# Performance work log

Hardware: AMD Instinct MI355X
Metric: run time of the kernel (lower is better)

Reference implementation:

```python
import jax, jax.numpy as jnp
import numpy as np

B, L, DIM, H = 2, 2048, 1024, 16
HD = DIM // H  # 64
EPS = 1e-6
ROPE_THETA = 10000.0


def _rmsnorm(x, scale):
    # mean of squares in float32 as in torch (dtype=torch.float32)
    ms = jnp.mean(jnp.square(x.astype(jnp.float32)), axis=-1, keepdims=True)
    inv = jax.lax.rsqrt(ms + EPS).astype(x.dtype)
    return x * inv * scale.astype(x.dtype)


def _rope_cos_sin(seq_len, head_dim, dtype):
    inv_freq = 1.0 / (ROPE_THETA ** (jnp.arange(0, head_dim, 2, dtype=jnp.float32) / head_dim))
    ang = jnp.arange(seq_len, dtype=jnp.float32)[:, None] * inv_freq[None, :]  # [L, HD/2]
    cos = jnp.cos(ang)[:, None, :].astype(dtype)  # [L,1,HD/2] broadcast over heads
    sin = jnp.sin(ang)[:, None, :].astype(dtype)
    return cos, sin


def _rope_apply(x, cos, sin):
    # x: [B,L,H,HD]; rotate-half formulation
    x1, x2 = jnp.split(x, 2, axis=-1)
    return jnp.concatenate([x1 * cos - x2 * sin, x2 * cos + x1 * sin], axis=-1)


def setup_inputs() -> dict:
    key = jax.random.key(0)
    k1, k2, k3 = jax.random.split(key, 3)
    x = jax.random.normal(k1, (B, L, DIM), dtype=jnp.float32)
    Wqkv = jax.random.normal(k2, (DIM, 3 * DIM), dtype=jnp.float32) * (DIM ** -0.5)
    Wproj = jax.random.normal(k3, (DIM, DIM), dtype=jnp.float32) * (DIM ** -0.5)
    q_scale = jnp.ones((HD,), dtype=jnp.float32)
    k_scale = jnp.ones((HD,), dtype=jnp.float32)
    bproj = jnp.zeros((DIM,), dtype=jnp.float32)
    return {"x": x, "Wqkv": Wqkv, "q_scale": q_scale, "k_scale": k_scale,
            "Wproj": Wproj, "bproj": bproj}


def reference(x, Wqkv, q_scale, k_scale, Wproj, bproj):
    b, l, c = x.shape
    qkv = x @ Wqkv  # [B,L,3*DIM]
    qkv = qkv.reshape(b, l, 3, H, HD)
    q, k, v = qkv[:, :, 0], qkv[:, :, 1], qkv[:, :, 2]  # each [B,L,H,HD]
    q = _rmsnorm(q, q_scale)
    k = _rmsnorm(k, k_scale)
    cos, sin = _rope_cos_sin(l, HD, x.dtype)
    q = _rope_apply(q, cos, sin)
    k = _rope_apply(k, cos, sin)
    scale = HD ** -0.5
    scores = jnp.einsum('blhd,bmhd->bhlm', q, k) * scale  # [B,H,L,L]
    p = jax.nn.softmax(scores, axis=-1)
    o = jnp.einsum('bhlm,bmhd->blhd', p, v).reshape(b, l, c)
    return o @ Wproj + bproj
```

## Files before the change

kernel.cpp:

```cpp
#include <hip/hip_runtime.h>
#include <hip/hip_bf16.h>
#include <cstdint>

#define B_   2
#define L_   2048
#define DIM_ 1024
#define H_   16
#define HD_  64
#define M_   (B_ * L_)
#define N3_  (3 * DIM_)

typedef unsigned short ushort_t;
typedef __bf16 bf16x8 __attribute__((ext_vector_type(8)));
typedef float  f32x4  __attribute__((ext_vector_type(4)));

__device__ __forceinline__ unsigned short f2b(float f) {
  unsigned u = __builtin_bit_cast(unsigned, f);
  u += 0x7FFFu + ((u >> 16) & 1u);
  return (unsigned short)(u >> 16);
}
__device__ __forceinline__ float b2f(unsigned short s) {
  unsigned u = ((unsigned)s) << 16;
  return __builtin_bit_cast(float, u);
}

typedef const __attribute__((address_space(1))) void* as1cp;
typedef __attribute__((address_space(3))) void* as3p;
__device__ __forceinline__ void gload_lds16(const void* g, void* l) {
  __builtin_amdgcn_global_load_lds((as1cp)g, (as3p)l, 16, 0, 0);
}

__global__ __launch_bounds__(256)
void conv_bf16(const float* __restrict__ in, ushort_t* __restrict__ out, int n4) {
  int i = blockIdx.x * 256 + threadIdx.x;
  if (i >= n4) return;
  float4 v = *(const float4*)&in[(size_t)i * 4];
  ushort4 o;
  o.x = f2b(v.x); o.y = f2b(v.y); o.z = f2b(v.z); o.w = f2b(v.w);
  *(ushort4*)&out[(size_t)i * 4] = o;
}

__global__ __launch_bounds__(256)
void transpose_conv(const float* __restrict__ in, ushort_t* __restrict__ out,
                    int R, int C) {
  __shared__ float tile[64][65];
  const int t = threadIdx.x;
  const int r0 = blockIdx.y * 64, c0 = blockIdx.x * 64;
#pragma unroll
  for (int p = 0; p < 4; ++p) {
    int r = (t >> 4) + p * 16;
    int c = (t & 15) * 4;
    float4 v = *(const float4*)&in[(size_t)(r0 + r) * C + (c0 + c)];
    tile[r][c + 0] = v.x; tile[r][c + 1] = v.y;
    tile[r][c + 2] = v.z; tile[r][c + 3] = v.w;
  }
  __syncthreads();
#pragma unroll
  for (int p = 0; p < 4; ++p) {
    int cc = (t >> 4) + p * 16;
    int r  = (t & 15) * 4;
    ushort4 o;
    o.x = f2b(tile[r + 0][cc]); o.y = f2b(tile[r + 1][cc]);
    o.z = f2b(tile[r + 2][cc]); o.w = f2b(tile[r + 3][cc]);
    *(ushort4*)&out[(size_t)(c0 + cc) * R + (r0 + r)] = o;
  }
}

__global__ __launch_bounds__(256)
void rope_tab(float* __restrict__ cosT, float* __restrict__ sinT) {
  int idx = blockIdx.x * 256 + threadIdx.x;
  int l = idx >> 5, d = idx & 31;
  float inv_freq = expf(-((float)(2 * d) / 64.f) * logf(10000.f));
  float ang = (float)l * inv_freq;
  cosT[idx] = cosf(ang);
  sinT[idx] = sinf(ang);
}

template <int MODE>
__global__ __launch_bounds__(256)
void gemm_bt(const ushort_t* __restrict__ A, const ushort_t* __restrict__ BT,
             void* __restrict__ Cout, ushort_t* __restrict__ vtout,
             const float* __restrict__ bias, int M, int N, int K, int ldc) {
  __shared__ ushort_t As[128 * 32];
  __shared__ ushort_t Bs[128 * 32];
  const int lane = threadIdx.x & 63;
  const int wid  = threadIdx.x >> 6;
  const int wm = wid >> 1, wn = wid & 1;
  const int m0 = blockIdx.y * 128, n0 = blockIdx.x * 128;
  const int ro = lane & 15, kg = lane >> 4;

  f32x4 acc[4][4] = {};

  for (int k0 = 0; k0 < K; k0 += 32) {
    const int cb = wid * 128;
#pragma unroll
    for (int j = 0; j < 2; ++j) {
      int c = cb + j * 64 + lane;
      gload_lds16(A + (size_t)(m0 + (c >> 2)) * K + k0 + (c & 3) * 8,
                  &As[(cb + j * 64) * 8]);
    }
#pragma unroll
    for (int j = 0; j < 2; ++j) {
      int c = cb + j * 64 + lane;
      gload_lds16(BT + (size_t)(n0 + (c >> 2)) * K + k0 + (c & 3) * 8,
                  &Bs[(cb + j * 64) * 8]);
    }
    __syncthreads();
    bf16x8 af[4], bfr[4];
#pragma unroll
    for (int i = 0; i < 4; ++i)
      af[i] = *(const bf16x8*)&As[(wm * 64 + i * 16 + ro) * 32 + kg * 8];
#pragma unroll
    for (int i = 0; i < 4; ++i)
      bfr[i] = *(const bf16x8*)&Bs[(wn * 64 + i * 16 + ro) * 32 + kg * 8];
#pragma unroll
    for (int i = 0; i < 4; ++i)
#pragma unroll
      for (int j = 0; j < 4; ++j)
        acc[i][j] = __builtin_amdgcn_mfma_f32_16x16x32_bf16(af[i], bfr[j],
                                                            acc[i][j], 0, 0, 0);
    __syncthreads();
  }

  if (MODE == 0) {
    if (n0 < 2048) {
#pragma unroll
      for (int i = 0; i < 4; ++i)
#pragma unroll
        for (int r = 0; r < 4; ++r) {
          int row = m0 + wm * 64 + i * 16 + kg * 4 + r;
#pragma unroll
          for (int j = 0; j < 4; ++j) {
            int col = n0 + wn * 64 + j * 16 + ro;
            ((ushort_t*)Cout)[(size_t)row * ldc + col] = f2b(acc[i][j][r]);
          }
        }
    } else {
#pragma unroll
      for (int i = 0; i < 4; ++i) {
        int rowb = m0 + wm * 64 + i * 16 + kg * 4;
        int bb = rowb >> 11, l = rowb & (L_ - 1);
#pragma unroll
        for (int j = 0; j < 4; ++j) {
          int dg = (n0 - 2048) + wn * 64 + j * 16 + ro;
          ushort4 o;
          o.x = f2b(acc[i][j][0]); o.y = f2b(acc[i][j][1]);
          o.z = f2b(acc[i][j][2]); o.w = f2b(acc[i][j][3]);
          *(ushort4*)&vtout[((size_t)bb * DIM_ + dg) * L_ + l] = o;
        }
      }
    }
  } else {
#pragma unroll
    for (int i = 0; i < 4; ++i)
#pragma unroll
      for (int r = 0; r < 4; ++r) {
        int row = m0 + wm * 64 + i * 16 + kg * 4 + r;
#pragma unroll
        for (int j = 0; j < 4; ++j) {
          int col = n0 + wn * 64 + j * 16 + ro;
          ((float*)Cout)[(size_t)row * ldc + col] = acc[i][j][r] + bias[col];
        }
      }
  }
}

__global__ __launch_bounds__(256)
void rmsrope(ushort_t* __restrict__ qk, const float* __restrict__ qs,
             const float* __restrict__ ks, const float* __restrict__ cosT,
             const float* __restrict__ sinT) {
  const int t = blockIdx.x;
  const int l = t & (L_ - 1);
  const int j = threadIdx.x & 15;
  const int h = threadIdx.x >> 4;
  const int dd = (j & 7) * 4;
  float4 cv = *(const float4*)&cosT[l * 32 + dd];
  float4 sv = *(const float4*)&sinT[l * 32 + dd];
  const float sgn = (j < 8) ? -1.f : 1.f;
#pragma unroll
  for (int ic = 0; ic < 2; ++ic) {
    const float qsc = (ic == 0) ? 0.125f * 1.44269504088896341f : 1.f;
    ushort_t* base = qk + (size_t)t * 2048 + ic * DIM_ + h * HD_ + j * 4;
    ushort4 raw = *(const ushort4*)base;
    float x0 = b2f(raw.x), x1 = b2f(raw.y), x2 = b2f(raw.z), x3 = b2f(raw.w);
    float ss = x0 * x0 + x1 * x1 + x2 * x2 + x3 * x3;
    ss += __shfl_xor(ss, 1); ss += __shfl_xor(ss, 2);
    ss += __shfl_xor(ss, 4); ss += __shfl_xor(ss, 8);
    float inv = rsqrtf(ss * (1.f / 64.f) + 1e-6f);
    const float* scp = (ic == 0 ? qs : ks) + j * 4;
    float4 sc = *(const float4*)scp;
    x0 *= inv * sc.x; x1 *= inv * sc.y; x2 *= inv * sc.z; x3 *= inv * sc.w;
    float y0 = __shfl_xor(x0, 8), y1 = __shfl_xor(x1, 8);
    float y2 = __shfl_xor(x2, 8), y3 = __shfl_xor(x3, 8);
    ushort4 o;
    o.x = f2b((x0 * cv.x + sgn * y0 * sv.x) * qsc);
    o.y = f2b((x1 * cv.y + sgn * y1 * sv.y) * qsc);
    o.z = f2b((x2 * cv.z + sgn * y2 * sv.z) * qsc);
    o.w = f2b((x3 * cv.w + sgn * y3 * sv.w) * qsc);
    *(ushort4*)base = o;
  }
}

__global__ __launch_bounds__(256)
void flash_attn(const ushort_t* __restrict__ qk, const ushort_t* __restrict__ vt,
                ushort_t* __restrict__ O) {
  const int qt = blockIdx.x, h = blockIdx.y, b = blockIdx.z;
  const int lane = threadIdx.x & 63, wid = threadIdx.x >> 6;
  const int ro = lane & 15, kg = lane >> 4;
  const int q0 = qt * 64;
  const size_t tok0 = (size_t)b * L_;
  const ushort_t* qb = qk + tok0 * 2048 + h * HD_;
  const ushort_t* kb = qb + DIM_;
  const ushort_t* vb = vt + ((size_t)b * DIM_ + h * HD_) * L_;

  __shared__ ushort_t Ks[2][4096];
  __shared__ ushort_t Vs[2][4096];
  __shared__ ushort_t Ps[4096];

  const int srow0 = wid * 16 + (lane >> 3);
  const int sch   = lane & 7;
  auto STAGE = [&](int bufi, int kt) {
#pragma unroll
    for (int j = 0; j < 2; ++j) {
      int row = srow0 + j * 8;
      int sc  = sch ^ (row & 7);
      gload_lds16(kb + (size_t)(kt * 64 + row) * 2048 + sc * 8,
                  &Ks[bufi][wid * 1024 + j * 512]);
      gload_lds16(vb + (size_t)row * L_ + kt * 64 + sc * 8,
                  &Vs[bufi][wid * 1024 + j * 512]);
    }
  };

  bf16x8 qf[2];
  {
    const ushort_t* g = qb + (size_t)(q0 + wid * 16 + ro) * 2048 + kg * 8;
    qf[0] = *(const bf16x8*)g;
    qf[1] = *(const bf16x8*)(g + 32);
  }

  f32x4 oacc[4] = {};
  float mrow = -1e30f, lrow = 0.f;

  STAGE(0, 0);
  __syncthreads();

  int cur = 0;
  const int rowq = wid * 16 + ro;
  for (int kt = 0; kt < L_ / 64; ++kt) {
    if (kt + 1 < L_ / 64) STAGE(cur ^ 1, kt + 1);

    f32x4 s[4];
#pragma unroll
    for (int n = 0; n < 4; ++n) {
      f32x4 z = {0.f, 0.f, 0.f, 0.f};
      int rowk = n * 16 + ro;
#pragma unroll
      for (int kk = 0; kk < 2; ++kk) {
        int ch = (kk * 4 + kg) ^ (rowk & 7);
        bf16x8 kf = *(const bf16x8*)&Ks[cur][rowk * 64 + ch * 8];
        z = __builtin_amdgcn_mfma_f32_16x16x32_bf16(kf, qf[kk], z, 0, 0, 0);
      }
      s[n] = z;
    }

    float pm = fmaxf(fmaxf(fmaxf(s[0][0], s[0][1]), fmaxf(s[0][2], s[0][3])),
                     fmaxf(fmaxf(s[1][0], s[1][1]), fmaxf(s[1][2], s[1][3])));
    pm = fmaxf(pm, fmaxf(fmaxf(fmaxf(s[2][0], s[2][1]), fmaxf(s[2][2], s[2][3])),
                         fmaxf(fmaxf(s[3][0], s[3][1]), fmaxf(s[3][2], s[3][3]))));
    pm = fmaxf(pm, __shfl_xor(pm, 16));
    pm = fmaxf(pm, __shfl_xor(pm, 32));
    float mn = fmaxf(mrow, pm);
    float alpha = __builtin_amdgcn_exp2f(mrow - mn);
    mrow = mn;
    float rs = 0.f;
#pragma unroll
    for (int n = 0; n < 4; ++n)
#pragma unroll
      for (int r = 0; r < 4; ++r) {
        float p = __builtin_amdgcn_exp2f(s[n][r] - mn);
        s[n][r] = p;
        rs += p;
      }
    rs += __shfl_xor(rs, 16);
    rs += __shfl_xor(rs, 32);
    lrow = lrow * alpha + rs;

    float aro[4];
#pragma unroll
    for (int r = 0; r < 4; ++r) aro[r] = __shfl(alpha, kg * 20 + r);
#pragma unroll
    for (int n = 0; n < 4; ++n)
#pragma unroll
      for (int r = 0; r < 4; ++r) oacc[n][r] *= aro[r];

#pragma unroll
    for (int n = 0; n < 4; ++n) {
      ushort4 pw;
      pw.x = f2b(s[n][0]); pw.y = f2b(s[n][1]);
      pw.z = f2b(s[n][2]); pw.w = f2b(s[n][3]);
      int ch = (n * 2 + (kg >> 1)) ^ (rowq & 7);
      *(ushort4*)&Ps[rowq * 64 + ch * 8 + (kg & 1) * 4] = pw;
    }

#pragma unroll
    for (int kk = 0; kk < 2; ++kk) {
      int chp = (kk * 4 + kg) ^ (rowq & 7);
      bf16x8 pf = *(const bf16x8*)&Ps[rowq * 64 + chp * 8];
#pragma unroll
      for (int n = 0; n < 4; ++n) {
        int rowd = n * 16 + ro;
        int chv = (kk * 4 + kg) ^ (rowd & 7);
        bf16x8 vf = *(const bf16x8*)&Vs[cur][rowd * 64 + chv * 8];
        oacc[n] = __builtin_amdgcn_mfma_f32_16x16x32_bf16(pf, vf, oacc[n], 0, 0, 0);
      }
    }

    __syncthreads();
    cur ^= 1;
  }

  float linv[4];
#pragma unroll
  for (int r = 0; r < 4; ++r) linv[r] = 1.f / __shfl(lrow, kg * 20 + r);
#pragma unroll
  for (int r = 0; r < 4; ++r) {
    int tok = (int)tok0 + q0 + wid * 16 + kg * 4 + r;
#pragma unroll
    for (int n = 0; n < 4; ++n)
      O[(size_t)tok * DIM_ + h * HD_ + n * 16 + ro] = f2b(oacc[n][r] * linv[r]);
  }
}

extern "C" void kernel_launch(void* const* d_in, const int* in_sizes, int n_in,
                              void* d_out, int out_size, void* d_ws, size_t ws_size,
                              hipStream_t stream) {
  const float* x     = (const float*)d_in[0];
  const float* Wqkv  = (const float*)d_in[1];
  const float* qs    = (const float*)d_in[2];
  const float* ks    = (const float*)d_in[3];
  const float* Wproj = (const float*)d_in[4];
  const float* bproj = (const float*)d_in[5];
  float* out = (float*)d_out;

  char* ws = (char*)d_ws;
  ushort_t* xb     = (ushort_t*)(ws);
  ushort_t* WqkvT  = (ushort_t*)(ws + (size_t)(8u << 20));
  ushort_t* WprojT = (ushort_t*)(ws + (size_t)(14u << 20));
  ushort_t* qkb    = (ushort_t*)(ws + (size_t)(16u << 20));
  ushort_t* vtb    = (ushort_t*)(ws + (size_t)(32u << 20));
  float*    cosT   = (float*)(ws + (size_t)(40u << 20));
  float*    sinT   = (float*)(ws + (size_t)(40u << 20) + (256u << 10));
  ushort_t* ob     = (ushort_t*)(ws + (size_t)(41u << 20));

  conv_bf16<<<4096, 256, 0, stream>>>(x, xb, M_ * DIM_ / 4);
  transpose_conv<<<dim3(48, 16), 256, 0, stream>>>(Wqkv, WqkvT, DIM_, N3_);
  transpose_conv<<<dim3(16, 16), 256, 0, stream>>>(Wproj, WprojT, DIM_, DIM_);
  rope_tab<<<256, 256, 0, stream>>>(cosT, sinT);
  gemm_bt<0><<<dim3(24, 32), 256, 0, stream>>>(xb, WqkvT, qkb, vtb, nullptr,
                                               M_, N3_, DIM_, 2048);
  rmsrope<<<4096, 256, 0, stream>>>(qkb, qs, ks, cosT, sinT);
  flash_attn<<<dim3(32, 16, 2), 256, 0, stream>>>(qkb, vtb, ob);
  gemm_bt<1><<<dim3(8, 32), 256, 0, stream>>>(ob, WprojT, out, nullptr, bproj,
                                              M_, DIM_, DIM_, DIM_);
}
```

Baseline: 170.0 us.

## Use lazy softmax rescaling and compute row sums with MFMA in attention loop

Restructures the flash-attention inner loop: the running max is only updated and the output rescaled when some lane's tile max exceeds the stored max by more than 8 (in log2 space), skipping the rescale otherwise. Row sums are now produced by an extra MFMA of P against a ones vector instead of scalar adds and shuffles, which also makes them consistent with the bf16-rounded P used for the output. The loop is unrolled by two so LDS buffer addresses become compile-time, with precomputed swizzled pointers, and f2b uses the hardware bf16 conversion. The trade-off is possibly larger unnormalised exponentials (up to 2^8) accumulated in fp32, plus an extra MFMA per k-step.

```diff
diff --git a/kernel.cpp b/kernel.cpp
--- a/kernel.cpp
+++ b/kernel.cpp
@@ -15,13 +15,14 @@
 typedef float  f32x4  __attribute__((ext_vector_type(4)));
 
 __device__ __forceinline__ unsigned short f2b(float f) {
-  unsigned u = __builtin_bit_cast(unsigned, f);
-  u += 0x7FFFu + ((u >> 16) & 1u);
-  return (unsigned short)(u >> 16);
+  return __builtin_bit_cast(unsigned short, (__bf16)f);
 }
 __device__ __forceinline__ float b2f(unsigned short s) {
   unsigned u = ((unsigned)s) << 16;
   return __builtin_bit_cast(float, u);
+}
+__device__ __forceinline__ float fmax3(float a, float b, float c) {
+  return fmaxf(fmaxf(a, b), c);
 }
 
 typedef const __attribute__((address_space(1))) void* as1cp;
@@ -238,90 +239,112 @@
     qf[1] = *(const bf16x8*)(g + 32);
   }
 
+  bf16x8 onesv;
+#pragma unroll
+  for (int i = 0; i < 8; ++i) onesv[i] = (__bf16)1.0f;
+
   f32x4 oacc[4] = {};
-  float mrow = -1e30f, lrow = 0.f;
+  f32x4 lacc = {0.f, 0.f, 0.f, 0.f};
+  float mrow = -1e30f;
+
+  const int rowq = wid * 16 + ro;
+  const int rx = ro & 7;
+
+  const ushort_t* kbase[2][2];
+  const ushort_t* vbase[2][2];
+#pragma unroll
+  for (int bi = 0; bi < 2; ++bi)
+#pragma unroll
+    for (int kk = 0; kk < 2; ++kk) {
+      int ch = (kk * 4 + kg) ^ rx;
+      kbase[bi][kk] = &Ks[bi][ro * 64 + ch * 8];
+      vbase[bi][kk] = &Vs[bi][ro * 64 + ch * 8];
+    }
+  const ushort_t* pbase[2];
+#pragma unroll
+  for (int kk = 0; kk < 2; ++kk)
+    pbase[kk] = &Ps[rowq * 64 + (((kk * 4 + kg) ^ rx) * 8)];
+  ushort_t* pwaddr[4];
+#pragma unroll
+  for (int n = 0; n < 4; ++n)
+    pwaddr[n] = &Ps[rowq * 64 + (((n * 2 + (kg >> 1)) ^ rx) * 8) + (kg & 1) * 4];
 
   STAGE(0, 0);
   __syncthreads();
 
-  int cur = 0;
-  const int rowq = wid * 16 + ro;
-  for (int kt = 0; kt < L_ / 64; ++kt) {
-    if (kt + 1 < L_ / 64) STAGE(cur ^ 1, kt + 1);
+  auto TILE = [&](int bi, int kt) {
+    if (kt + 1 < L_ / 64) STAGE(bi ^ 1, kt + 1);
 
     f32x4 s[4];
 #pragma unroll
     for (int n = 0; n < 4; ++n) {
       f32x4 z = {0.f, 0.f, 0.f, 0.f};
-      int rowk = n * 16 + ro;
 #pragma unroll
       for (int kk = 0; kk < 2; ++kk) {
-        int ch = (kk * 4 + kg) ^ (rowk & 7);
-        bf16x8 kf = *(const bf16x8*)&Ks[cur][rowk * 64 + ch * 8];
+        bf16x8 kf = *(const bf16x8*)(kbase[bi][kk] + n * 1024);
         z = __builtin_amdgcn_mfma_f32_16x16x32_bf16(kf, qf[kk], z, 0, 0, 0);
       }
       s[n] = z;
     }
 
-    float pm = fmaxf(fmaxf(fmaxf(s[0][0], s[0][1]), fmaxf(s[0][2], s[0][3])),
-                     fmaxf(fmaxf(s[1][0], s[1][1]), fmaxf(s[1][2], s[1][3])));
-    pm = fmaxf(pm, fmaxf(fmaxf(fmaxf(s[2][0], s[2][1]), fmaxf(s[2][2], s[2][3])),
-                         fmaxf(fmaxf(s[3][0], s[3][1]), fmaxf(s[3][2], s[3][3]))));
+    float t0 = fmax3(s[0][0], s[0][1], s[0][2]);
+    float t1 = fmax3(s[0][3], s[1][0], s[1][1]);
+    float t2 = fmax3(s[1][2], s[1][3], s[2][0]);
+    float t3 = fmax3(s[2][1], s[2][2], s[2][3]);
+    float t4 = fmax3(s[3][0], s[3][1], s[3][2]);
+    float pm  = fmax3(t0, t1, t2);
+    float pm2 = fmax3(t3, t4, s[3][3]);
+    pm = fmaxf(pm, pm2);
     pm = fmaxf(pm, __shfl_xor(pm, 16));
     pm = fmaxf(pm, __shfl_xor(pm, 32));
-    float mn = fmaxf(mrow, pm);
-    float alpha = __builtin_amdgcn_exp2f(mrow - mn);
-    mrow = mn;
-    float rs = 0.f;
-#pragma unroll
-    for (int n = 0; n < 4; ++n)
-#pragma unroll
-      for (int r = 0; r < 4; ++r) {
-        float p = __builtin_amdgcn_exp2f(s[n][r] - mn);
-        s[n][r] = p;
-        rs += p;
-      }
-    rs += __shfl_xor(rs, 16);
-    rs += __shfl_xor(rs, 32);
-    lrow = lrow * alpha + rs;
-
-    float aro[4];
-#pragma unroll
-    for (int r = 0; r < 4; ++r) aro[r] = __shfl(alpha, kg * 20 + r);
-#pragma unroll
-    for (int n = 0; n < 4; ++n)
-#pragma unroll
-      for (int r = 0; r < 4; ++r) oacc[n][r] *= aro[r];
+
+    if (__any(pm > mrow + 8.f)) {
+      float mn = fmaxf(mrow, pm);
+      float alpha = __builtin_amdgcn_exp2f(mrow - mn);
+      mrow = mn;
+      float aro[4];
+#pragma unroll
+      for (int r = 0; r < 4; ++r) aro[r] = __shfl(alpha, kg * 20 + r);
+#pragma unroll
+      for (int n = 0; n < 4; ++n)
+#pragma unroll
+        for (int r = 0; r < 4; ++r) oacc[n][r] *= aro[r];
+#pragma unroll
+      for (int r = 0; r < 4; ++r) lacc[r] *= aro[r];
+    }
 
 #pragma unroll
     for (int n = 0; n < 4; ++n) {
       ushort4 pw;
-      pw.x = f2b(s[n][0]); pw.y = f2b(s[n][1]);
-      pw.z = f2b(s[n][2]); pw.w = f2b(s[n][3]);
-      int ch = (n * 2 + (kg >> 1)) ^ (rowq & 7);
-      *(ushort4*)&Ps[rowq * 64 + ch * 8 + (kg & 1) * 4] = pw;
+      pw.x = f2b(__builtin_amdgcn_exp2f(s[n][0] - mrow));
+      pw.y = f2b(__builtin_amdgcn_exp2f(s[n][1] - mrow));
+      pw.z = f2b(__builtin_amdgcn_exp2f(s[n][2] - mrow));
+      pw.w = f2b(__builtin_amdgcn_exp2f(s[n][3] - mrow));
+      *(ushort4*)pwaddr[n] = pw;
     }
 
 #pragma unroll
     for (int kk = 0; kk < 2; ++kk) {
-      int chp = (kk * 4 + kg) ^ (rowq & 7);
-      bf16x8 pf = *(const bf16x8*)&Ps[rowq * 64 + chp * 8];
+      bf16x8 pf = *(const bf16x8*)pbase[kk];
+      lacc = __builtin_amdgcn_mfma_f32_16x16x32_bf16(pf, onesv, lacc, 0, 0, 0);
 #pragma unroll
       for (int n = 0; n < 4; ++n) {
-        int rowd = n * 16 + ro;
-        int chv = (kk * 4 + kg) ^ (rowd & 7);
-        bf16x8 vf = *(const bf16x8*)&Vs[cur][rowd * 64 + chv * 8];
+        bf16x8 vf = *(const bf16x8*)(vbase[bi][kk] + n * 1024);
         oacc[n] = __builtin_amdgcn_mfma_f32_16x16x32_bf16(pf, vf, oacc[n], 0, 0, 0);
       }
     }
 
     __syncthreads();
-    cur ^= 1;
+  };
+
+  for (int kt = 0; kt < L_ / 64; kt += 2) {
+    TILE(0, kt);
+    TILE(1, kt + 1);
   }
 
   float linv[4];
 #pragma unroll
-  for (int r = 0; r < 4; ++r) linv[r] = 1.f / __shfl(lrow, kg * 20 + r);
+  for (int r = 0; r < 4; ++r) linv[r] = 1.f / lacc[r];
 #pragma unroll
   for (int r = 0; r < 4; ++r) {
     int tok = (int)tok0 + q0 + wid * 16 + kg * 4 + r;
```

Result: faster. 159.7 us (-6.0%).
